# Kernel optimization log

Hardware: AMD Instinct MI355X
Metric: run time of the kernel (lower is better)

The kernel has to match this reference:

```python
import jax, jax.numpy as jnp
import numpy as np
import itertools

RANK = 2  # window size per axis; mode='linear' -> stride 1; rank_op='avg'; rank_mode='drop'


def setup_inputs() -> dict:
    key = jax.random.key(0)
    k1, k2, k3 = jax.random.split(key, 3)
    m = 32
    D = 20
    hypervol = jax.random.normal(k1, (D, D, D, D, m), dtype=jnp.float32)
    # nn.Linear weight init U(-0.5, 0.5); P init U(-0.1, 0.1)
    M_w = jax.random.uniform(k2, (m, m), dtype=jnp.float32, minval=-0.5, maxval=0.5)
    P = jax.random.uniform(k3, (m, m), dtype=jnp.float32, minval=-0.1, maxval=0.1)
    return {"hypervol": hypervol, "M_w": M_w, "P": P}


def reference(hypervol, M_w, P):
    m = P.shape[0]
    D1, D2, D3, D4, _ = hypervol.shape
    o1, o2, o3, o4 = D1 - RANK + 1, D2 - RANK + 1, D3 - RANK + 1, D4 - RANK + 1

    # Vectorized window extraction with mean reduction ('avg'):
    # mean over RANK^4 window = average of RANK^4 shifted slices (fixed small loop).
    acc = jnp.zeros((o1, o2, o3, o4, m), dtype=hypervol.dtype)
    for a, b, c, d in itertools.product(range(RANK), repeat=4):
        acc = acc + hypervol[a:a + o1, b:b + o2, c:c + o3, d:d + o4, :]
    win = acc / float(RANK ** 4)  # [o1,o2,o3,o4,m]

    # M(v): Linear without bias -> v @ W^T
    x = jnp.einsum('abcdj,ij->abcdi', win, M_w)  # [o1,o2,o3,o4,m]
    # note: output index of Linear is i; below x plays role of (M v) with einsum index j
    x = jnp.einsum('abcdi->abcdi', x)  # no-op, keep shape clear

    # periods[i,j] = i*m + j + 2 (identical for all four axes)
    ii = jnp.arange(m, dtype=jnp.float32)
    periods = ii[:, None] * m + ii[None, :] + 2.0  # [m,m]
    two_pi = jnp.float32(2.0 * np.pi)

    def ctab(n):
        k = jnp.arange(n, dtype=jnp.float32)
        return jnp.cos(two_pi * k[:, None, None] / periods)  # [n,m,m]

    C1, C2, C3, C4 = ctab(o1), ctab(o2), ctab(o3), ctab(o4)
    # phi[a,b,c,d,i,j] = C1[a]*C2[b]*C3[c]*C4[d]; built from tiny per-axis tables
    phi = (C1[:, None, None, None] * C2[None, :, None, None]) \
          [:, :, :, None] * 0.0  # placeholder removed below
    phi = (C1[:, None, None, None, :, :]
           * C2[None, :, None, None, :, :]
           * C3[None, None, :, None, :, :]
           * C4[None, None, None, :, :, :])  # [o1,o2,o3,o4,m,m]

    # N(k)_i = sum_j P_ij * (Mv)_j * phi_ij  (matches einsum 'bj,ij,bij->bi')
    Nk = jnp.einsum('abcdj,ij,abcdij->abcdi', x, P, phi)
    return Nk.reshape(-1, m)  # [num_windows, m], window order = k1-major like the loops
```

## Files before the change

kernel.cpp:

```cpp
#include <hip/hip_runtime.h>

#define DD 20
#define MM 32
#define OO 19
#define NWIN (OO*OO*OO)
#define WPB 4
#define NBLK ((NWIN + WPB - 1) / WPB)

#define CS_FLOATS (OO*MM*MM)
#define PS_OFF CS_FLOATS
#define MS_OFF (PS_OFF + MM*MM)
#define WS_FLOATS (MS_OFF + MM*MM)

#define LSLICE 1248
#define WOFF 640

__global__ __launch_bounds__(256) void build_tables_kernel(
        const float* __restrict__ Mw, const float* __restrict__ P,
        float* __restrict__ ws) {
    const int idx = blockIdx.x * 256 + threadIdx.x;
    if (idx < CS_FLOATS) {
        const int k    = idx >> 10;
        const int r    = idx & 1023;
        const int q    = r >> 8;
        const int lane = (r >> 2) & 63;
        const int e    = r & 3;
        const int i    = lane & 31;
        const int j    = (lane >> 5) * 16 + q * 4 + e;
        const float period = (float)(i * MM + j + 2);
        ws[idx] = cosf(6.28318530717958647692f * (float)k / period);
    } else if (idx < WS_FLOATS) {
        const int r    = (idx - PS_OFF) & 1023;
        const int q    = r >> 8;
        const int lane = (r >> 2) & 63;
        const int e    = r & 3;
        const int i    = lane & 31;
        const int j    = (lane >> 5) * 16 + q * 4 + e;
        ws[idx] = (idx < MS_OFF) ? P[i * MM + j]
                                 : Mw[i * MM + j] * 0.0625f;
    }
}

__device__ __forceinline__ void lds_sync() {
    __builtin_amdgcn_s_waitcnt(0xC07F);
    __builtin_amdgcn_wave_barrier();
}

__global__ __launch_bounds__(256, 4) void spatial_kernel(
        const float* __restrict__ H, const float* __restrict__ ws,
        float* __restrict__ out) {
    __shared__ __align__(16) float sLDS[WPB][LSLICE];

    const int tid  = threadIdx.x;
    const int w    = tid >> 6;
    const int lane = tid & 63;
    const int i    = lane & 31;
    const int h    = lane >> 5;
    const int jb   = h * 16;

    const int raw = blockIdx.x;
    const int xcd = raw & 7;
    const int k   = raw >> 3;
    const int sb  = (xcd < 3) ? (xcd * 215 + k) : (645 + (xcd - 3) * 214 + k);
    const int win = sb * WPB + w;
    if (win >= NWIN) return;
    const int c = win % OO;
    const int b = (win / OO) % OO;
    const int a = win / (OO * OO);

    const float4* __restrict__ T = (const float4*)ws;
    float* __restrict__ S = sLDS[w];
    float* __restrict__ W = sLDS[w] + WOFF;
    float* __restrict__ X = sLDS[w];

    float mt[16];
    #pragma unroll
    for (int q = 0; q < 4; ++q) {
        const float4 v = T[(MS_OFF >> 2) + q * 64 + lane];
        mt[q*4+0] = v.x; mt[q*4+1] = v.y; mt[q*4+2] = v.z; mt[q*4+3] = v.w;
    }

    {
        float4 a0 = make_float4(0.f, 0.f, 0.f, 0.f);
        float4 a1 = a0, a2 = a0;
        #pragma unroll
        for (int da = 0; da < 2; ++da)
            #pragma unroll
            for (int db = 0; db < 2; ++db)
                #pragma unroll
                for (int dc = 0; dc < 2; ++dc) {
                    const float4* __restrict__ p = (const float4*)(
                        H + (size_t)((((a + da) * DD + (b + db)) * DD + (c + dc)) * DD) * MM);
                    const float4 v0 = p[lane];
                    const float4 v1 = p[64 + lane];
                    a0.x += v0.x; a0.y += v0.y; a0.z += v0.z; a0.w += v0.w;
                    a1.x += v1.x; a1.y += v1.y; a1.z += v1.z; a1.w += v1.w;
                    if (lane < 32) {
                        const float4 v2 = p[128 + lane];
                        a2.x += v2.x; a2.y += v2.y; a2.z += v2.z; a2.w += v2.w;
                    }
                }
        ((float4*)S)[lane]      = a0;
        ((float4*)S)[64 + lane] = a1;
        if (lane < 32) ((float4*)S)[128 + lane] = a2;
    }
    lds_sync();

    #pragma unroll
    for (int t = 0; t < 10; ++t) {
        const int idx = t * 64 + lane;
        if (idx < OO * MM)
            W[idx] = S[idx] + S[idx + MM];
    }
    lds_sync();

    #pragma unroll
    for (int d = 0; d < OO; ++d) {
        const float4* __restrict__ wr = (const float4*)(W + d * MM + jb);
        float t = 0.f;
        #pragma unroll
        for (int q = 0; q < 4; ++q) {
            const float4 v = wr[q];
            t += v.x * mt[q*4+0] + v.y * mt[q*4+1]
               + v.z * mt[q*4+2] + v.w * mt[q*4+3];
        }
        t += __shfl_xor(t, 32, 64);
        if (h == 0) X[d * MM + i] = t;
    }
    lds_sync();

    float s0[16], s1[16], t2c[16];
    #pragma unroll
    for (int q = 0; q < 4; ++q) {
        const float4 pv = T[(PS_OFF >> 2) + q * 64 + lane];
        const float4 va = T[(a * 4 + q) * 64 + lane];
        const float4 vb = T[(b * 4 + q) * 64 + lane];
        const float4 vc = T[(c * 4 + q) * 64 + lane];
        const float4 c1 = T[(1 * 4 + q) * 64 + lane];
        const float qpx = pv.x * va.x * vb.x * vc.x;
        const float qpy = pv.y * va.y * vb.y * vc.y;
        const float qpz = pv.z * va.z * vb.z * vc.z;
        const float qpw = pv.w * va.w * vb.w * vc.w;
        s1[q*4+0] = qpx; s0[q*4+0] = qpx * c1.x; t2c[q*4+0] = c1.x + c1.x;
        s1[q*4+1] = qpy; s0[q*4+1] = qpy * c1.y; t2c[q*4+1] = c1.y + c1.y;
        s1[q*4+2] = qpz; s0[q*4+2] = qpz * c1.z; t2c[q*4+2] = c1.z + c1.z;
        s1[q*4+3] = qpw; s0[q*4+3] = qpw * c1.w; t2c[q*4+3] = c1.w + c1.w;
    }
    const size_t obase = (size_t)win * (OO * MM);
    #pragma unroll
    for (int d = 0; d < OO; ++d) {
        const float4* __restrict__ xr = (const float4*)(X + d * MM + jb);
        float t = 0.f;
        #pragma unroll
        for (int q = 0; q < 4; ++q) {
            const float4 v = xr[q];
            t += v.x * s1[q*4+0] + v.y * s1[q*4+1]
               + v.z * s1[q*4+2] + v.w * s1[q*4+3];
        }
        #pragma unroll
        for (int jj = 0; jj < 16; ++jj) {
            const float nx = __builtin_fmaf(t2c[jj], s1[jj], -s0[jj]);
            s0[jj] = s1[jj];
            s1[jj] = nx;
        }
        t += __shfl_xor(t, 32, 64);
        if (h == 0) out[obase + d * MM + i] = t;
    }
}

extern "C" void kernel_launch(void* const* d_in, const int* in_sizes, int n_in,
                              void* d_out, int out_size, void* d_ws, size_t ws_size,
                              hipStream_t stream) {
    const float* H  = (const float*)d_in[0];
    const float* Mw = (const float*)d_in[1];
    const float* P  = (const float*)d_in[2];
    float* out = (float*)d_out;
    float* ws  = (float*)d_ws;

    build_tables_kernel<<<WS_FLOATS / 256, 256, 0, stream>>>(Mw, P, ws);
    spatial_kernel<<<NBLK, 256, 0, stream>>>(H, ws, out);
}
```

Baseline: 95.31 us.

## Process two adjacent c-windows per wave to share hypervolume loads

Each wave now handles a pair of neighbouring windows along the c axis (ten tasks per (a,b) row, the last one unpaired). The three consecutive c-slices are loaded once and summed into two partial windows, so the shared middle slice is read one time instead of twice. The wave also reuses the a*b*P product and overlaps the second window's reduction with the first window's output phase. The trade-off is more LDS per wave, more registers and half as many waves, which may lower occupancy and parallelism.

```diff
diff --git a/kernel.cpp b/kernel.cpp
--- a/kernel.cpp
+++ b/kernel.cpp
@@ -4,16 +4,21 @@
 #define MM 32
 #define OO 19
 #define NWIN (OO*OO*OO)
+#define TPAB 10
+#define NTASK (OO*OO*TPAB)
 #define WPB 4
-#define NBLK ((NWIN + WPB - 1) / WPB)
+#define NBLK ((NTASK + WPB - 1) / WPB)
 
 #define CS_FLOATS (OO*MM*MM)
 #define PS_OFF CS_FLOATS
 #define MS_OFF (PS_OFF + MM*MM)
 #define WS_FLOATS (MS_OFF + MM*MM)
 
-#define LSLICE 1248
-#define WOFF 640
+#define LSLICE 1888
+#define S2OFF 640
+#define WOFF 1280
+
+#define ACC4(d, s) { (d).x += (s).x; (d).y += (s).y; (d).z += (s).z; (d).w += (s).w; }
 
 __global__ __launch_bounds__(256) void build_tables_kernel(
         const float* __restrict__ Mw, const float* __restrict__ P,
@@ -60,111 +65,164 @@
 
     const int raw = blockIdx.x;
     const int xcd = raw & 7;
-    const int k   = raw >> 3;
-    const int sb  = (xcd < 3) ? (xcd * 215 + k) : (645 + (xcd - 3) * 214 + k);
-    const int win = sb * WPB + w;
-    if (win >= NWIN) return;
-    const int c = win % OO;
-    const int b = (win / OO) % OO;
-    const int a = win / (OO * OO);
+    const int kk  = raw >> 3;
+    const int sb  = (xcd < 7) ? (xcd * 113 + kk) : (791 + kk);
+    const int task = sb * WPB + w;
+    if (task >= NTASK) return;
+
+    const int q  = task % TPAB;
+    const int ab = task / TPAB;
+    const int b  = ab % OO;
+    const int a  = ab / OO;
+    const int c  = q * 2;
+    const bool paired = (q < 9);
+    const int win1 = (a * OO + b) * OO + c;
 
     const float4* __restrict__ T = (const float4*)ws;
-    float* __restrict__ S = sLDS[w];
-    float* __restrict__ W = sLDS[w] + WOFF;
-    float* __restrict__ X = sLDS[w];
+    float* __restrict__ S1 = sLDS[w];
+    float* __restrict__ S2 = sLDS[w] + S2OFF;
+    float* __restrict__ W  = sLDS[w] + WOFF;
+    float* __restrict__ X1 = sLDS[w];
+    float* __restrict__ X2 = sLDS[w] + S2OFF;
 
     float mt[16];
     #pragma unroll
-    for (int q = 0; q < 4; ++q) {
-        const float4 v = T[(MS_OFF >> 2) + q * 64 + lane];
-        mt[q*4+0] = v.x; mt[q*4+1] = v.y; mt[q*4+2] = v.z; mt[q*4+3] = v.w;
+    for (int qq = 0; qq < 4; ++qq) {
+        const float4 v = T[(MS_OFF >> 2) + qq * 64 + lane];
+        mt[qq*4+0] = v.x; mt[qq*4+1] = v.y; mt[qq*4+2] = v.z; mt[qq*4+3] = v.w;
     }
 
     {
-        float4 a0 = make_float4(0.f, 0.f, 0.f, 0.f);
-        float4 a1 = a0, a2 = a0;
+        float4 a10 = make_float4(0.f, 0.f, 0.f, 0.f);
+        float4 a11 = a10, a12 = a10;
+        float4 a20 = a10, a21 = a10, a22 = a10;
         #pragma unroll
         for (int da = 0; da < 2; ++da)
             #pragma unroll
-            for (int db = 0; db < 2; ++db)
-                #pragma unroll
-                for (int dc = 0; dc < 2; ++dc) {
-                    const float4* __restrict__ p = (const float4*)(
-                        H + (size_t)((((a + da) * DD + (b + db)) * DD + (c + dc)) * DD) * MM);
-                    const float4 v0 = p[lane];
-                    const float4 v1 = p[64 + lane];
-                    a0.x += v0.x; a0.y += v0.y; a0.z += v0.z; a0.w += v0.w;
-                    a1.x += v1.x; a1.y += v1.y; a1.z += v1.z; a1.w += v1.w;
-                    if (lane < 32) {
-                        const float4 v2 = p[128 + lane];
-                        a2.x += v2.x; a2.y += v2.y; a2.z += v2.z; a2.w += v2.w;
+            for (int db = 0; db < 2; ++db) {
+                const float* rb = H + (size_t)((((a + da) * DD + (b + db)) * DD + c) * DD) * MM;
+                const float4* __restrict__ p0 = (const float4*)rb;
+                const float4* __restrict__ p1 = (const float4*)(rb + DD * MM);
+                const float4* __restrict__ p2 = (const float4*)(rb + 2 * DD * MM);
+                const float4 u0 = p0[lane],      u1 = p0[64 + lane];
+                const float4 v0 = p1[lane],      v1 = p1[64 + lane];
+                ACC4(a10, u0); ACC4(a10, v0);
+                ACC4(a11, u1); ACC4(a11, v1);
+                if (paired) {
+                    const float4 t0 = p2[lane], t1 = p2[64 + lane];
+                    ACC4(a20, v0); ACC4(a20, t0);
+                    ACC4(a21, v1); ACC4(a21, t1);
+                }
+                if (lane < 32) {
+                    const float4 u2 = p0[128 + lane], v2 = p1[128 + lane];
+                    ACC4(a12, u2); ACC4(a12, v2);
+                    if (paired) {
+                        const float4 t2 = p2[128 + lane];
+                        ACC4(a22, v2); ACC4(a22, t2);
                     }
                 }
-        ((float4*)S)[lane]      = a0;
-        ((float4*)S)[64 + lane] = a1;
-        if (lane < 32) ((float4*)S)[128 + lane] = a2;
+            }
+        float4* s1v = (float4*)S1;
+        s1v[lane] = a10; s1v[64 + lane] = a11;
+        if (lane < 32) s1v[128 + lane] = a12;
+        if (paired) {
+            float4* s2v = (float4*)S2;
+            s2v[lane] = a20; s2v[64 + lane] = a21;
+            if (lane < 32) s2v[128 + lane] = a22;
+        }
     }
     lds_sync();
 
+    auto p15 = [&](const float* __restrict__ Sx) {
+        #pragma unroll
+        for (int t = 0; t < 10; ++t) {
+            const int idx = t * 64 + lane;
+            if (idx < OO * MM)
+                W[idx] = Sx[idx] + Sx[idx + MM];
+        }
+    };
+
+    auto p2f = [&](float* __restrict__ Xx) {
+        #pragma unroll
+        for (int d = 0; d < OO; ++d) {
+            const float4* __restrict__ wr = (const float4*)(W + d * MM + jb);
+            float t = 0.f;
+            #pragma unroll
+            for (int qq = 0; qq < 4; ++qq) {
+                const float4 v = wr[qq];
+                t += v.x * mt[qq*4+0] + v.y * mt[qq*4+1]
+                   + v.z * mt[qq*4+2] + v.w * mt[qq*4+3];
+            }
+            t += __shfl_xor(t, 32, 64);
+            if (h == 0) Xx[d * MM + i] = t;
+        }
+    };
+
+    p15(S1);
+    lds_sync();
+    p2f(X1);
+    lds_sync();
+
+    float qab[16], s0[16], s1[16], t2c[16];
     #pragma unroll
-    for (int t = 0; t < 10; ++t) {
-        const int idx = t * 64 + lane;
-        if (idx < OO * MM)
-            W[idx] = S[idx] + S[idx + MM];
-    }
-    lds_sync();
-
-    #pragma unroll
-    for (int d = 0; d < OO; ++d) {
-        const float4* __restrict__ wr = (const float4*)(W + d * MM + jb);
-        float t = 0.f;
-        #pragma unroll
-        for (int q = 0; q < 4; ++q) {
-            const float4 v = wr[q];
-            t += v.x * mt[q*4+0] + v.y * mt[q*4+1]
-               + v.z * mt[q*4+2] + v.w * mt[q*4+3];
-        }
-        t += __shfl_xor(t, 32, 64);
-        if (h == 0) X[d * MM + i] = t;
-    }
-    lds_sync();
-
-    float s0[16], s1[16], t2c[16];
-    #pragma unroll
-    for (int q = 0; q < 4; ++q) {
-        const float4 pv = T[(PS_OFF >> 2) + q * 64 + lane];
-        const float4 va = T[(a * 4 + q) * 64 + lane];
-        const float4 vb = T[(b * 4 + q) * 64 + lane];
-        const float4 vc = T[(c * 4 + q) * 64 + lane];
-        const float4 c1 = T[(1 * 4 + q) * 64 + lane];
-        const float qpx = pv.x * va.x * vb.x * vc.x;
-        const float qpy = pv.y * va.y * vb.y * vc.y;
-        const float qpz = pv.z * va.z * vb.z * vc.z;
-        const float qpw = pv.w * va.w * vb.w * vc.w;
-        s1[q*4+0] = qpx; s0[q*4+0] = qpx * c1.x; t2c[q*4+0] = c1.x + c1.x;
-        s1[q*4+1] = qpy; s0[q*4+1] = qpy * c1.y; t2c[q*4+1] = c1.y + c1.y;
-        s1[q*4+2] = qpz; s0[q*4+2] = qpz * c1.z; t2c[q*4+2] = c1.z + c1.z;
-        s1[q*4+3] = qpw; s0[q*4+3] = qpw * c1.w; t2c[q*4+3] = c1.w + c1.w;
-    }
-    const size_t obase = (size_t)win * (OO * MM);
-    #pragma unroll
-    for (int d = 0; d < OO; ++d) {
-        const float4* __restrict__ xr = (const float4*)(X + d * MM + jb);
-        float t = 0.f;
-        #pragma unroll
-        for (int q = 0; q < 4; ++q) {
-            const float4 v = xr[q];
-            t += v.x * s1[q*4+0] + v.y * s1[q*4+1]
-               + v.z * s1[q*4+2] + v.w * s1[q*4+3];
-        }
-        #pragma unroll
-        for (int jj = 0; jj < 16; ++jj) {
-            const float nx = __builtin_fmaf(t2c[jj], s1[jj], -s0[jj]);
-            s0[jj] = s1[jj];
-            s1[jj] = nx;
-        }
-        t += __shfl_xor(t, 32, 64);
-        if (h == 0) out[obase + d * MM + i] = t;
+    for (int qq = 0; qq < 4; ++qq) {
+        const float4 pv = T[(PS_OFF >> 2) + qq * 64 + lane];
+        const float4 va = T[(a * 4 + qq) * 64 + lane];
+        const float4 vb = T[(b * 4 + qq) * 64 + lane];
+        const float4 vc = T[(c * 4 + qq) * 64 + lane];
+        const float4 c1 = T[(1 * 4 + qq) * 64 + lane];
+        const float qx = pv.x * va.x * vb.x;
+        const float qy = pv.y * va.y * vb.y;
+        const float qz = pv.z * va.z * vb.z;
+        const float qw = pv.w * va.w * vb.w;
+        qab[qq*4+0] = qx; s1[qq*4+0] = qx * vc.x; s0[qq*4+0] = s1[qq*4+0] * c1.x; t2c[qq*4+0] = c1.x + c1.x;
+        qab[qq*4+1] = qy; s1[qq*4+1] = qy * vc.y; s0[qq*4+1] = s1[qq*4+1] * c1.y; t2c[qq*4+1] = c1.y + c1.y;
+        qab[qq*4+2] = qz; s1[qq*4+2] = qz * vc.z; s0[qq*4+2] = s1[qq*4+2] * c1.z; t2c[qq*4+2] = c1.z + c1.z;
+        qab[qq*4+3] = qw; s1[qq*4+3] = qw * vc.w; s0[qq*4+3] = s1[qq*4+3] * c1.w; t2c[qq*4+3] = c1.w + c1.w;
+    }
+
+    auto p3f = [&](const float* __restrict__ Xx, size_t obase) {
+        #pragma unroll
+        for (int d = 0; d < OO; ++d) {
+            const float4* __restrict__ xr = (const float4*)(Xx + d * MM + jb);
+            float t = 0.f;
+            #pragma unroll
+            for (int qq = 0; qq < 4; ++qq) {
+                const float4 v = xr[qq];
+                t += v.x * s1[qq*4+0] + v.y * s1[qq*4+1]
+                   + v.z * s1[qq*4+2] + v.w * s1[qq*4+3];
+            }
+            #pragma unroll
+            for (int jj = 0; jj < 16; ++jj) {
+                const float nx = __builtin_fmaf(t2c[jj], s1[jj], -s0[jj]);
+                s0[jj] = s1[jj];
+                s1[jj] = nx;
+            }
+            t += __shfl_xor(t, 32, 64);
+            if (h == 0) out[obase + d * MM + i] = t;
+        }
+    };
+
+    float4 vc2[4];
+    if (paired) {
+        #pragma unroll
+        for (int qq = 0; qq < 4; ++qq)
+            vc2[qq] = T[((c + 1) * 4 + qq) * 64 + lane];
+        p15(S2);
+    }
+    p3f(X1, (size_t)win1 * (OO * MM));
+    if (paired) {
+        lds_sync();
+        #pragma unroll
+        for (int qq = 0; qq < 4; ++qq) {
+            s1[qq*4+0] = qab[qq*4+0] * vc2[qq].x; s0[qq*4+0] = s1[qq*4+0] * (0.5f * t2c[qq*4+0]);
+            s1[qq*4+1] = qab[qq*4+1] * vc2[qq].y; s0[qq*4+1] = s1[qq*4+1] * (0.5f * t2c[qq*4+1]);
+            s1[qq*4+2] = qab[qq*4+2] * vc2[qq].z; s0[qq*4+2] = s1[qq*4+2] * (0.5f * t2c[qq*4+2]);
+            s1[qq*4+3] = qab[qq*4+3] * vc2[qq].w; s0[qq*4+3] = s1[qq*4+3] * (0.5f * t2c[qq*4+3]);
+        }
+        p2f(X2);
+        lds_sync();
+        p3f(X2, (size_t)(win1 + 1) * (OO * MM));
     }
 }
 
```

Result: slower. 98.19 us (+3.0%).
